# Optimization experiments

Measured on AMD Instinct MI355X. Metric: run time of the kernel, lower is better.

The kernel has to match this reference:

```python
import jax, jax.numpy as jnp
import numpy as np

# --- static config ---
B = 64        # graphs per batch
NPG = 512     # nodes per graph
N = B * NPG   # total nodes = 32768
EPG = 8192    # edges per graph (avg degree 16)
E = B * EPG   # total edges = 524288
L = 16        # tokens per node
V = 50000     # vocab
H = 256       # hidden_size == rnn hidden_size
P = 128       # projection_dim
K1 = 256      # ceil(0.5 * 512) nodes kept after pool 1
K2 = 128      # ceil(0.5 * 256) nodes kept after pool 2
PAD = 0


def setup_inputs() -> dict:
    key = jax.random.key(0)
    ks = jax.random.split(key, 16)
    tokens = jax.random.randint(ks[0], (N, L), 0, V, dtype=jnp.int32)
    eg = jnp.repeat(jnp.arange(B, dtype=jnp.int32), EPG)  # graph id per edge
    src = jax.random.randint(ks[1], (E,), 0, NPG, dtype=jnp.int32) + eg * NPG
    dst = jax.random.randint(ks[2], (E,), 0, NPG, dtype=jnp.int32) + eg * NPG
    edge_attr = jax.random.uniform(ks[3], (E, 2), dtype=jnp.float32)
    sH = 1.0 / np.sqrt(H).astype(np.float32)
    sP = 1.0 / np.sqrt(P).astype(np.float32)
    return {
        'tokens': tokens, 'src': src, 'dst': dst, 'edge_attr': edge_attr,
        'emb': jax.random.normal(ks[4], (V, H), jnp.float32) * 0.05,
        'W0': jax.random.normal(ks[5], (H, H), jnp.float32) * sH,
        'b0': jnp.zeros((H,), jnp.float32),
        'W1': jax.random.normal(ks[6], (H, H), jnp.float32) * sH,
        'b1': jnp.zeros((H,), jnp.float32),
        'p0': jax.random.normal(ks[7], (H,), jnp.float32),
        'p1': jax.random.normal(ks[8], (H,), jnp.float32),
        'wg': jax.random.normal(ks[9], (H, 1), jnp.float32) * sH,
        'bg': jnp.zeros((1,), jnp.float32),
        'Wp1': jax.random.normal(ks[10], (H, P), jnp.float32) * sH,
        'bp1': jnp.zeros((P,), jnp.float32),
        'Wp2': jax.random.normal(ks[11], (P, P), jnp.float32) * sP,
        'bp2': jnp.zeros((P,), jnp.float32),
    }


def _st_encode(tokens, emb):
    # STEncoder proxy: embed token ids, masked mean over non-pad tokens -> [N, H]
    mask = (tokens != PAD).astype(jnp.float32)  # [N, L]
    e = emb[tokens] * mask[..., None]           # [N, L, H]
    cnt = jnp.maximum(mask.sum(-1, keepdims=True), 1.0)
    return e.sum(1) / cnt


def _gcn(x, W, b, src, dst, w, n):
    # GCNConv with edge weights + self loops (fill 1), symmetric normalization
    h = x @ W                                        # [n, H]
    deg = jax.ops.segment_sum(w, dst, num_segments=n) + 1.0
    dinv = jax.lax.rsqrt(deg)
    norm = dinv[src] * w * dinv[dst]                 # [E]
    agg = jax.ops.segment_sum(h[src] * norm[:, None], dst, num_segments=n)
    return agg + h * (1.0 / deg)[:, None] + b


def _topk_pool(x, p, src, dst, w, n_per, k):
    # TopKPooling: score = x.p/||p||, keep top-k per graph, gate by tanh(score)
    G = x.shape[0] // n_per
    score = (x @ p) / jnp.linalg.norm(p)
    vals, idx = jax.lax.top_k(score.reshape(G, n_per), k)   # [G, k]
    perm = (idx + (jnp.arange(G, dtype=jnp.int32) * n_per)[:, None]).reshape(-1)
    x_new = x[perm] * jnp.tanh(vals.reshape(-1))[:, None]
    new_of_old = jnp.full((G * n_per,), -1, jnp.int32).at[perm].set(
        jnp.arange(G * k, dtype=jnp.int32))
    ns, nd = new_of_old[src], new_of_old[dst]
    keep = (ns >= 0) & (nd >= 0)
    # masked edges: weight 0 -> contribute nothing (== subgraph filtering)
    return (x_new, jnp.where(keep, ns, 0), jnp.where(keep, nd, 0),
            jnp.where(keep, w, 0.0))


def _attpool(x, wg, bg, k):
    # GlobalAttention: softmax(Linear(x,1)) over each graph's nodes
    G = x.shape[0] // k
    gate = (x @ wg + bg).reshape(G, k)        # [G, k]
    a = jax.nn.softmax(gate, axis=1)
    return jnp.einsum('gk,gkh->gh', a, x.reshape(G, k, x.shape[-1]))


def reference(tokens, src, dst, edge_attr, emb, W0, b0, W1, b1, p0, p1,
              wg, bg, Wp1, bp1, Wp2, bp2):
    w = edge_attr.mean(axis=1)                 # GCN path: scalar edge weights
    x = _st_encode(tokens, emb)                # [N, H]
    # layer 1
    x = jax.nn.relu(_gcn(x, W0, b0, src, dst, w, N))
    x, src1, dst1, w1 = _topk_pool(x, p0, src, dst, w, NPG, K1)
    out = _attpool(x, wg, bg, K1)              # [B, H]
    # hidden layer
    x = jax.nn.relu(_gcn(x, W1, b1, src1, dst1, w1, B * K1))
    x, _, _, _ = _topk_pool(x, p1, src1, dst1, w1, K1, K2)
    out = out + _attpool(x, wg, bg, K2)
    # projection head + L2 normalize
    h = jax.nn.relu(out @ Wp1 + bp1)
    logits = h @ Wp2 + bp2
    logits = logits / jnp.maximum(
        jnp.linalg.norm(logits, axis=-1, keepdims=True), 1e-12)
    return (logits, out)
```

## Files before the change

### kernel.cpp

```cpp
#include <hip/hip_runtime.h>
#include <hip/hip_bf16.h>

constexpr int C_B   = 64;
constexpr int C_NPG = 512;
constexpr int C_N   = 32768;
constexpr int C_E   = 524288;
constexpr int C_L   = 16;
constexpr int C_H   = 256;
constexpr int C_P   = 128;
constexpr int C_K1  = 256;
constexpr int C_K2  = 128;
constexpr int C_V   = 50000;

typedef __attribute__((ext_vector_type(8)))  short  short8;
typedef __attribute__((ext_vector_type(16))) float  float16;
typedef unsigned short ushort;
typedef unsigned int   uint;

__device__ inline void split_bf16(float x, ushort& h, ushort& l) {
    __hip_bfloat16 bh = __float2bfloat16(x);
    float fh = __bfloat162float(bh);
    __hip_bfloat16 bl = __float2bfloat16(x - fh);
    h = __builtin_bit_cast(ushort, bh);
    l = __builtin_bit_cast(ushort, bl);
}

__device__ inline ushort f2h(float x) {
    return __builtin_bit_cast(ushort, (_Float16)x);
}
__device__ inline float4 h4_to_f4(ushort4 v) {
    return make_float4((float)__builtin_bit_cast(_Float16, v.x),
                       (float)__builtin_bit_cast(_Float16, v.y),
                       (float)__builtin_bit_cast(_Float16, v.z),
                       (float)__builtin_bit_cast(_Float16, v.w));
}

template <int NPER>
__device__ inline void bitonic_desc(float& v, int& idx, float* svL, int* siL, int t) {
    #pragma unroll
    for (int k = 2; k <= NPER; k <<= 1) {
        bool desc = ((t & k) == 0);
        #pragma unroll
        for (int j = k >> 1; j > 0; j >>= 1) {
            bool amLo = ((t & j) == 0);
            bool keepMax = (desc == amLo);
            float pv; int pi;
            if (j >= 64) {
                __syncthreads();
                svL[t] = v; siL[t] = idx;
                __syncthreads();
                pv = svL[t ^ j]; pi = siL[t ^ j];
            } else {
                pv = __shfl_xor(v, j, 64);
                pi = __shfl_xor(idx, j, 64);
            }
            bool take = keepMax ? (pv > v) : (pv < v);
            if (take) { v = pv; idx = pi; }
        }
    }
}

__global__ void k_pre(const float* __restrict__ emb, ushort* __restrict__ emb16,
                      const float* __restrict__ ea, const int* __restrict__ dst,
                      float* __restrict__ w, float* __restrict__ degb, int* __restrict__ indegb,
                      const float* __restrict__ W0, const float* __restrict__ W1,
                      ushort* __restrict__ W0h, ushort* __restrict__ W0l,
                      ushort* __restrict__ W1h, ushort* __restrict__ W1l,
                      const float* __restrict__ p0, const float* __restrict__ p1,
                      float* __restrict__ invnp) {
    int b = blockIdx.x, t = threadIdx.x;
    __shared__ float r[256];
    if (b < 6250) {
        int i = (b * 256 + t) * 8;
        float4 a = *(const float4*)&emb[i];
        float4 c = *(const float4*)&emb[i + 4];
        short8 o;
        o[0] = (short)f2h(a.x); o[1] = (short)f2h(a.y);
        o[2] = (short)f2h(a.z); o[3] = (short)f2h(a.w);
        o[4] = (short)f2h(c.x); o[5] = (short)f2h(c.y);
        o[6] = (short)f2h(c.z); o[7] = (short)f2h(c.w);
        *(short8*)&emb16[i] = o;
    } else if (b < 8298) {
        int e = (b - 6250) * 256 + t;
        float ww = 0.5f * (ea[2 * e] + ea[2 * e + 1]);
        w[e] = ww;
        int d = dst[e];
        atomicAdd(&degb[d], ww);
        atomicAdd(&indegb[d], 1);
    } else if (b < 8810) {
        int g = (b - 8298) * 256 + t;
        int which = g >> 16;
        int idx = g & 65535;
        int k = idx >> 8, n = idx & 255;
        float x = (which ? W1 : W0)[idx];
        ushort h, l;
        split_bf16(x, h, l);
        size_t a = ((size_t)(n >> 5) * 16 + (k >> 4)) * 512 + ((k >> 3) & 1) * 256
                 + (n & 31) * 8 + (k & 7);
        if (which) { W1h[a] = h; W1l[a] = l; }
        else       { W0h[a] = h; W0l[a] = l; }
    } else {
        const float* p = (b == 8810) ? p0 : p1;
        float v = p[t];
        r[t] = v * v; __syncthreads();
        for (int s = 128; s; s >>= 1) { if (t < s) r[t] += r[t + s]; __syncthreads(); }
        if (t == 0) invnp[b - 8810] = rsqrtf(r[0]);
    }
}

template <int NPER>
__global__ void k_scan(const int* __restrict__ indeg, int* __restrict__ rowstart,
                       int* __restrict__ cursor, float* __restrict__ deg,
                       float* __restrict__ dinv) {
    int g = blockIdx.x, t = threadIdx.x;
    int node = g * NPER + t;
    float d = deg[node] + 1.f;
    dinv[node] = rsqrtf(d);
    deg[node]  = 1.f / d;
    __shared__ int s[NPER];
    int v = indeg[node];
    s[t] = v;
    __syncthreads();
    for (int off = 1; off < NPER; off <<= 1) {
        int add = (t >= off) ? s[t - off] : 0;
        __syncthreads();
        s[t] += add;
        __syncthreads();
    }
    int start = g * 8192 + s[t] - v;
    rowstart[node] = start;
    cursor[node]   = start;
}

__global__ void k_csr_scatter(const int* __restrict__ src, const int* __restrict__ dst,
                              const float* __restrict__ w, const float* __restrict__ dinv,
                              int* __restrict__ cursor, int* __restrict__ csr_src,
                              float* __restrict__ csr_nrm) {
    int e = blockIdx.x * blockDim.x + threadIdx.x;
    if (e >= C_E) return;
    int s = src[e], d = dst[e];
    int slot = atomicAdd(&cursor[d], 1);
    csr_src[slot] = s;
    csr_nrm[slot] = dinv[s] * w[e] * dinv[d];
}

__global__ __launch_bounds__(256)
void k_gcn_gather(const ushort* __restrict__ Hm, const int* __restrict__ rowstart,
                  const int* __restrict__ indeg, const int* __restrict__ csr_src,
                  const float* __restrict__ csr_nrm, const float* __restrict__ selfw,
                  const float* __restrict__ bias, const float* __restrict__ p,
                  const float* __restrict__ invnp, float* __restrict__ Xout,
                  float* __restrict__ score, int nnodes) {
    int n    = (blockIdx.x * blockDim.x + threadIdx.x) >> 6;
    int lane = threadIdx.x & 63;
    if (n >= nnodes) return;
    int h4 = lane * 4;
    float4 hv = h4_to_f4(*(const ushort4*)&Hm[(size_t)n * C_H + h4]);
    float  sw = selfw[n];
    float4 bv = *(const float4*)&bias[h4];
    float4 acc = make_float4(fmaf(hv.x, sw, bv.x), fmaf(hv.y, sw, bv.y),
                             fmaf(hv.z, sw, bv.z), fmaf(hv.w, sw, bv.w));
    int start = rowstart[n], cnt = indeg[n];
    const int*   sp = csr_src + start;
    const float* np = csr_nrm + start;
    #pragma unroll 4
    for (int j = 0; j < cnt; ++j) {
        int   s  = sp[j];
        float nm = np[j];
        float4 xv = h4_to_f4(*(const ushort4*)&Hm[(size_t)s * C_H + h4]);
        acc.x = fmaf(nm, xv.x, acc.x);
        acc.y = fmaf(nm, xv.y, acc.y);
        acc.z = fmaf(nm, xv.z, acc.z);
        acc.w = fmaf(nm, xv.w, acc.w);
    }
    acc.x = fmaxf(acc.x, 0.f); acc.y = fmaxf(acc.y, 0.f);
    acc.z = fmaxf(acc.z, 0.f); acc.w = fmaxf(acc.w, 0.f);
    *(float4*)&Xout[(size_t)n * C_H + h4] = acc;
    float4 pv = *(const float4*)&p[h4];
    float s = acc.x * pv.x + acc.y * pv.y + acc.z * pv.z + acc.w * pv.w;
    #pragma unroll
    for (int m = 32; m; m >>= 1) s += __shfl_xor(s, m, 64);
    if (lane == 0) score[n] = s * invnp[0];
}

__global__ __launch_bounds__(256)
void k_st_encode4(const int* __restrict__ tokens, const ushort* __restrict__ emb16,
                  ushort* __restrict__ Xh, ushort* __restrict__ Xl) {
    __shared__ float Xs[32 * 257];
    __shared__ int tokS[512];
    int tid = threadIdx.x;
    int blk = blockIdx.x;
    tokS[tid]       = tokens[(size_t)blk * 512 + tid];
    tokS[tid + 256] = tokens[(size_t)blk * 512 + tid + 256];
    __syncthreads();
    int w    = tid >> 6;
    int lane = tid & 63;
    for (int i = 0; i < 8; ++i) {
        int nl = w * 8 + i;
        float4 acc = make_float4(0.f, 0.f, 0.f, 0.f);
        int cnt = 0;
        #pragma unroll
        for (int t = 0; t < C_L; ++t) {
            int tk = tokS[nl * 16 + t];
            if (tk != 0) {
                float4 ev = h4_to_f4(*(const ushort4*)&emb16[(size_t)tk * C_H + lane * 4]);
                acc.x += ev.x; acc.y += ev.y; acc.z += ev.z; acc.w += ev.w;
                cnt++;
            }
        }
        float inv = 1.f / fmaxf((float)cnt, 1.f);
        float* xr = &Xs[nl * 257 + lane * 4];
        xr[0] = acc.x * inv; xr[1] = acc.y * inv;
        xr[2] = acc.z * inv; xr[3] = acc.w * inv;
    }
    __syncthreads();
    #pragma unroll
    for (int i = 0; i < 4; ++i) {
        int c    = tid + 256 * i;
        int kst  = c >> 6;
        int ln   = c & 63;
        int ml   = ln & 31;
        int kb   = kst * 16 + (ln >> 5) * 8;
        short8 hv, lv;
        #pragma unroll
        for (int j = 0; j < 8; ++j) {
            ushort h, l;
            split_bf16(Xs[ml * 257 + kb + j], h, l);
            hv[j] = (short)h; lv[j] = (short)l;
        }
        size_t base = (size_t)blk * 8192 + (size_t)c * 8;
        *(short8*)&Xh[base] = hv;
        *(short8*)&Xl[base] = lv;
    }
}

__global__ __launch_bounds__(256)
void k_gemm_mfma(const ushort* __restrict__ Ah, const ushort* __restrict__ Al,
                 const ushort* __restrict__ Bh, const ushort* __restrict__ Bl,
                 ushort* __restrict__ C) {
    __shared__ short lds[16384];
    int tid  = threadIdx.x;
    int lane = tid & 63;
    int wid  = tid >> 6;
    int wm   = wid & 1, wn = wid >> 1;
    int mb   = blockIdx.x;
    int nb   = blockIdx.y;

    float16 acc[2][2];
    #pragma unroll
    for (int mi = 0; mi < 2; ++mi)
        #pragma unroll
        for (int ni = 0; ni < 2; ++ni)
            #pragma unroll
            for (int r = 0; r < 16; ++r) acc[mi][ni][r] = 0.f;

    for (int kc = 0; kc < 8; ++kc) {
        __syncthreads();
        #pragma unroll
        for (int i = 0; i < 4; ++i) {
            int a  = tid + 256 * i;
            int s  = a >> 9;
            int mt = (a >> 7) & 3;
            int k2 = (a >> 6) & 1;
            int ln = a & 63;
            const ushort* ap = (s ? Al : Ah)
                + (((size_t)(mb * 4 + mt) * 16 + kc * 2 + k2) * 64 + ln) * 8;
            *(int4*)&lds[a * 8] = *(const int4*)ap;
            const ushort* bp = (s ? Bl : Bh)
                + (((size_t)(nb * 4 + mt) * 16 + kc * 2 + k2) * 64 + ln) * 8;
            *(int4*)&lds[8192 + a * 8] = *(const int4*)bp;
        }
        __syncthreads();
        #pragma unroll
        for (int k2 = 0; k2 < 2; ++k2) {
            short8 ah[2], al[2], bh[2], bl[2];
            #pragma unroll
            for (int mi = 0; mi < 2; ++mi) {
                int mt = wm * 2 + mi;
                ah[mi] = *(short8*)&lds[((mt * 2 + k2) * 64 + lane) * 8];
                al[mi] = *(short8*)&lds[(((4 + mt) * 2 + k2) * 64 + lane) * 8];
            }
            #pragma unroll
            for (int ni = 0; ni < 2; ++ni) {
                int nt = wn * 2 + ni;
                bh[ni] = *(short8*)&lds[8192 + ((nt * 2 + k2) * 64 + lane) * 8];
                bl[ni] = *(short8*)&lds[8192 + (((4 + nt) * 2 + k2) * 64 + lane) * 8];
            }
            #pragma unroll
            for (int mi = 0; mi < 2; ++mi)
                #pragma unroll
                for (int ni = 0; ni < 2; ++ni) {
                    acc[mi][ni] = __builtin_amdgcn_mfma_f32_32x32x16_bf16(
                        ah[mi], bh[ni], acc[mi][ni], 0, 0, 0);
                    acc[mi][ni] = __builtin_amdgcn_mfma_f32_32x32x16_bf16(
                        ah[mi], bl[ni], acc[mi][ni], 0, 0, 0);
                    acc[mi][ni] = __builtin_amdgcn_mfma_f32_32x32x16_bf16(
                        al[mi], bh[ni], acc[mi][ni], 0, 0, 0);
                }
        }
    }
    int col = lane & 31;
    int rquad = 4 * (lane >> 5);
    #pragma unroll
    for (int mi = 0; mi < 2; ++mi)
        #pragma unroll
        for (int ni = 0; ni < 2; ++ni) {
            int mbase = mb * 128 + wm * 64 + mi * 32;
            int nbase = nb * 128 + wn * 64 + ni * 32 + col;
            #pragma unroll
            for (int r = 0; r < 16; ++r) {
                int row = (r & 3) + 8 * (r >> 2) + rquad;
                C[(size_t)(mbase + row) * C_H + nbase] = f2h(acc[mi][ni][r]);
            }
        }
}

__global__ __launch_bounds__(512)
void k_pool1_fused(const float* __restrict__ score, const float* __restrict__ X,
                   const int* __restrict__ src, const int* __restrict__ dst,
                   const float* __restrict__ wbuf,
                   const float* __restrict__ wg, const float* __restrict__ bg,
                   ushort* __restrict__ XFh, ushort* __restrict__ XFl,
                   float* __restrict__ outb,
                   float* __restrict__ selfw1, int* __restrict__ rowst1,
                   int* __restrict__ indeg1, int* __restrict__ csrs,
                   float* __restrict__ csrn) {
    int g = blockIdx.x, t = threadIdx.x;
    int lane = t & 63, w = t >> 6;
    __shared__ float svL[C_NPG];
    __shared__ int   siL[C_NPG];
    __shared__ int   nooL[C_NPG];
    __shared__ int   olds[C_K1];
    __shared__ float gt[C_K1];
    __shared__ float sd[C_K1];
    __shared__ float red[C_K1];
    __shared__ float an[C_K1];
    __shared__ float wsum[8][C_H];
    __shared__ int   indegL[C_K1];
    __shared__ float degL[C_K1];
    __shared__ float dinvL[C_K1];
    __shared__ int   cursL[C_K1];

    float v = score[g * C_NPG + t];
    int   idx = t;
    bitonic_desc<C_NPG>(v, idx, svL, siL, t);
    __syncthreads();
    nooL[idx] = (t < C_K1) ? t : -1;
    if (t < C_K1) {
        olds[t]   = idx;
        gt[t]     = tanhf(v);
        indegL[t] = 0;
        degL[t]   = 0.f;
    }
    __syncthreads();

    float bgv = bg[0];
    {
        int r = t >> 1, half = t & 1;
        const float* xr = &X[(size_t)(g * C_NPG + olds[r]) * C_H + half * 128];
        const float* wr = &wg[half * 128];
        float s = 0.f;
        #pragma unroll
        for (int kk = 0; kk < 128; kk += 4) {
            float4 xv = *(const float4*)&xr[kk];
            float4 wv = *(const float4*)&wr[kk];
            s += xv.x * wv.x + xv.y * wv.y + xv.z * wv.z + xv.w * wv.w;
        }
        if (half) red[r] = s;
        __syncthreads();
        if (!half) sd[r] = gt[r] * (s + red[r]) + bgv;
        __syncthreads();
    }
    if (w == 0) {
        float m = fmaxf(fmaxf(sd[lane], sd[lane + 64]), fmaxf(sd[lane + 128], sd[lane + 192]));
        #pragma unroll
        for (int mm = 32; mm; mm >>= 1) m = fmaxf(m, __shfl_xor(m, mm, 64));
        if (lane == 0) red[0] = m;
    }
    __syncthreads();
    float mx = red[0];
    if (t < C_K1) an[t] = expf(sd[t] - mx);
    __syncthreads();
    if (w == 0) {
        float s4 = an[lane] + an[lane + 64] + an[lane + 128] + an[lane + 192];
        #pragma unroll
        for (int mm = 32; mm; mm >>= 1) s4 += __shfl_xor(s4, mm, 64);
        if (lane == 0) red[1] = s4;
    }
    __syncthreads();
    if (t < C_K1) an[t] = an[t] / red[1] * gt[t];
    __syncthreads();
    {
        float4 a4 = make_float4(0.f, 0.f, 0.f, 0.f);
        #pragma unroll 4
        for (int r = 0; r < 32; ++r) {
            int rr = w * 32 + r;
            float a = an[rr];
            float4 xv = *(const float4*)&X[(size_t)(g * C_NPG + olds[rr]) * C_H + lane * 4];
            a4.x = fmaf(a, xv.x, a4.x); a4.y = fmaf(a, xv.y, a4.y);
            a4.z = fmaf(a, xv.z, a4.z); a4.w = fmaf(a, xv.w, a4.w);
        }
        *(float4*)&wsum[w][lane * 4] = a4;
        __syncthreads();
        if (t < C_H) {
            float s = wsum[0][t] + wsum[1][t] + wsum[2][t] + wsum[3][t]
                    + wsum[4][t] + wsum[5][t] + wsum[6][t] + wsum[7][t];
            outb[g * C_H + t] = s;
        }
    }

    #pragma unroll
    for (int i = 0; i < 16; ++i) {
        int u   = t + 512 * i;
        int mt  = u >> 10;
        int c   = u & 1023;
        int kst = c >> 6, ln = c & 63, ml = ln & 31;
        int kb  = kst * 16 + (ln >> 5) * 8;
        int r   = mt * 32 + ml;
        const float* xp = &X[(size_t)(g * C_NPG + olds[r]) * C_H + kb];
        float gg = gt[r];
        float4 a = *(const float4*)&xp[0];
        float4 b = *(const float4*)&xp[4];
        float e8[8] = {a.x * gg, a.y * gg, a.z * gg, a.w * gg,
                       b.x * gg, b.y * gg, b.z * gg, b.w * gg};
        short8 hv, lv;
        #pragma unroll
        for (int j = 0; j < 8; ++j) {
            ushort h, l;
            split_bf16(e8[j], h, l);
            hv[j] = (short)h; lv[j] = (short)l;
        }
        size_t base = (size_t)(g * 8 + mt) * 8192 + (size_t)c * 8;
        *(short8*)&XFh[base] = hv;
        *(short8*)&XFl[base] = lv;
    }

    int   nsR[16], ndR[16];
    float wwR[16];
    #pragma unroll
    for (int i = 0; i < 16; ++i) {
        int e  = g * 8192 + t + 512 * i;
        int ns = nooL[src[e] - g * C_NPG];
        int nd = nooL[dst[e] - g * C_NPG];
        float ww = wbuf[e];
        nsR[i] = ns; ndR[i] = nd; wwR[i] = ww;
        if (ns >= 0 && nd >= 0) {
            atomicAdd(&indegL[nd], 1);
            unsafeAtomicAdd(&degL[nd], ww);
        }
    }
    __syncthreads();
    if (t < C_K1) {
        float d = degL[t] + 1.f;
        dinvL[t] = rsqrtf(d);
        selfw1[g * C_K1 + t] = 1.f / d;
        indeg1[g * C_K1 + t] = indegL[t];
    }
    if (w == 0) {
        int a0 = indegL[lane * 4], a1 = indegL[lane * 4 + 1];
        int a2 = indegL[lane * 4 + 2], a3 = indegL[lane * 4 + 3];
        int s4 = a0 + a1 + a2 + a3;
        int sc = s4;
        #pragma unroll
        for (int off = 1; off < 64; off <<= 1) {
            int pv = __shfl_up(sc, off, 64);
            if (lane >= off) sc += pv;
        }
        int base = g * 8192 + (sc - s4);
        cursL[lane * 4]     = base;
        cursL[lane * 4 + 1] = base + a0;
        cursL[lane * 4 + 2] = base + a0 + a1;
        cursL[lane * 4 + 3] = base + a0 + a1 + a2;
        rowst1[g * C_K1 + lane * 4]     = base;
        rowst1[g * C_K1 + lane * 4 + 1] = base + a0;
        rowst1[g * C_K1 + lane * 4 + 2] = base + a0 + a1;
        rowst1[g * C_K1 + lane * 4 + 3] = base + a0 + a1 + a2;
    }
    __syncthreads();
    #pragma unroll
    for (int i = 0; i < 16; ++i) {
        int ns = nsR[i], nd = ndR[i];
        if (ns >= 0 && nd >= 0) {
            int slot = atomicAdd(&cursL[nd], 1);
            csrs[slot] = g * C_K1 + ns;
            csrn[slot] = dinvL[ns] * wwR[i] * dinvL[nd];
        }
    }
}

__global__ __launch_bounds__(256)
void k_pool2_fused(const float* __restrict__ score, const float* __restrict__ X,
                   const float* __restrict__ wg, const float* __restrict__ bg,
                   float* __restrict__ outb) {
    int g = blockIdx.x, t = threadIdx.x;
    int lane = t & 63, w = t >> 6;
    __shared__ float svL[C_K1];
    __shared__ int   siL[C_K1];
    __shared__ int   olds[C_K2];
    __shared__ float gt[C_K2];
    __shared__ float sd[C_K2];
    __shared__ float red[C_K2];
    __shared__ float an[C_K2];
    __shared__ float wsum[4][C_H];

    float v = score[g * C_K1 + t];
    int   idx = t;
    bitonic_desc<C_K1>(v, idx, svL, siL, t);
    __syncthreads();
    if (t < C_K2) { olds[t] = idx; gt[t] = tanhf(v); }
    __syncthreads();

    float bgv = bg[0];
    {
        int r = t >> 1, half = t & 1;
        const float* xr = &X[(size_t)(g * C_K1 + olds[r]) * C_H + half * 128];
        const float* wr = &wg[half * 128];
        float s = 0.f;
        #pragma unroll
        for (int kk = 0; kk < 128; kk += 4) {
            float4 xv = *(const float4*)&xr[kk];
            float4 wv = *(const float4*)&wr[kk];
            s += xv.x * wv.x + xv.y * wv.y + xv.z * wv.z + xv.w * wv.w;
        }
        if (half) red[r] = s;
        __syncthreads();
        if (!half) sd[r] = gt[r] * (s + red[r]) + bgv;
        __syncthreads();
    }
    if (w == 0) {
        float m = fmaxf(sd[lane], sd[lane + 64]);
        #pragma unroll
        for (int mm = 32; mm; mm >>= 1) m = fmaxf(m, __shfl_xor(m, mm, 64));
        if (lane == 0) red[0] = m;
    }
    __syncthreads();
    float mx = red[0];
    if (t < C_K2) an[t] = expf(sd[t] - mx);
    __syncthreads();
    if (w == 0) {
        float s2 = an[lane] + an[lane + 64];
        #pragma unroll
        for (int mm = 32; mm; mm >>= 1) s2 += __shfl_xor(s2, mm, 64);
        if (lane == 0) red[1] = s2;
    }
    __syncthreads();
    if (t < C_K2) an[t] = an[t] / red[1] * gt[t];
    __syncthreads();
    {
        float4 a4 = make_float4(0.f, 0.f, 0.f, 0.f);
        #pragma unroll 4
        for (int r = 0; r < 32; ++r) {
            int rr = w * 32 + r;
            float a = an[rr];
            float4 xv = *(const float4*)&X[(size_t)(g * C_K1 + olds[rr]) * C_H + lane * 4];
            a4.x = fmaf(a, xv.x, a4.x); a4.y = fmaf(a, xv.y, a4.y);
            a4.z = fmaf(a, xv.z, a4.z); a4.w = fmaf(a, xv.w, a4.w);
        }
        *(float4*)&wsum[w][lane * 4] = a4;
        __syncthreads();
        float s = wsum[0][t] + wsum[1][t] + wsum[2][t] + wsum[3][t];
        outb[g * C_H + t] += s;
    }
}

__global__ void k_head(const float* __restrict__ outb, const float* __restrict__ Wp1,
                       const float* __restrict__ bp1, const float* __restrict__ Wp2,
                       const float* __restrict__ bp2, float* __restrict__ dout) {
    int g = blockIdx.x;
    int t = threadIdx.x;
    __shared__ float so[C_H];
    so[t] = outb[g * C_H + t];
    so[t + 128] = outb[g * C_H + t + 128];
    __syncthreads();
    float acc = bp1[t];
    for (int k = 0; k < C_H; ++k) acc += so[k] * Wp1[k * C_P + t];
    float hv = fmaxf(acc, 0.f);
    __shared__ float sh[C_P];
    sh[t] = hv; __syncthreads();
    float lg = bp2[t];
    for (int k = 0; k < C_P; ++k) lg += sh[k] * Wp2[k * C_P + t];
    __shared__ float red[C_P];
    red[t] = lg * lg; __syncthreads();
    for (int s = 64; s > 0; s >>= 1) { if (t < s) red[t] += red[t + s]; __syncthreads(); }
    float nrm = fmaxf(sqrtf(red[0]), 1e-12f);
    dout[g * C_P + t] = lg / nrm;
    dout[C_B * C_P + g * C_H + t]       = so[t];
    dout[C_B * C_P + g * C_H + t + 128] = so[t + 128];
}

extern "C" void kernel_launch(void* const* d_in, const int* in_sizes, int n_in,
                              void* d_out, int out_size, void* d_ws, size_t ws_size,
                              hipStream_t stream) {
    const int*   tokens = (const int*)d_in[0];
    const int*   src    = (const int*)d_in[1];
    const int*   dst    = (const int*)d_in[2];
    const float* eattr  = (const float*)d_in[3];
    const float* emb    = (const float*)d_in[4];
    const float* W0     = (const float*)d_in[5];
    const float* b0     = (const float*)d_in[6];
    const float* W1     = (const float*)d_in[7];
    const float* b1     = (const float*)d_in[8];
    const float* p0     = (const float*)d_in[9];
    const float* p1     = (const float*)d_in[10];
    const float* wg     = (const float*)d_in[11];
    const float* bg     = (const float*)d_in[12];
    const float* Wp1    = (const float*)d_in[13];
    const float* bp1    = (const float*)d_in[14];
    const float* Wp2    = (const float*)d_in[15];
    const float* bp2    = (const float*)d_in[16];
    float* out = (float*)d_out;

    float* f = (float*)d_ws;
    size_t o = 0;
    float*  XB    = f + o; o += (size_t)C_N * C_H;
    float*  HB    = f + o; o += (size_t)C_N * C_H;
    ushort* XFh   = (ushort*)(f + o); o += (size_t)C_N * C_H / 2;
    ushort* XFl   = (ushort*)(f + o); o += (size_t)C_N * C_H / 2;
    float*  wbuf  = f + o; o += C_E;
    float*  degb  = f + o; o += C_N;
    int*    indegb= (int*)(f + o); o += C_N;
    float*  dinv  = f + o; o += C_N;
    int*    rowst = (int*)(f + o); o += C_N;
    int*    curs  = (int*)(f + o); o += C_N;
    int*    csrs  = (int*)(f + o); o += C_E;
    float*  csrn  = f + o; o += C_E;
    float*  deg1  = f + o; o += C_B * C_K1;
    int*    indeg1= (int*)(f + o); o += C_B * C_K1;
    int*    rowst1= (int*)(f + o); o += C_B * C_K1;
    float*  outb  = f + o; o += C_B * C_H;
    float*  score = f + o; o += C_N;
    float*  invnp = f + o; o += 16;
    ushort* W0h   = (ushort*)(f + o); o += C_H * C_H / 2;
    ushort* W0l   = (ushort*)(f + o); o += C_H * C_H / 2;
    ushort* W1h   = (ushort*)(f + o); o += C_H * C_H / 2;
    ushort* W1l   = (ushort*)(f + o); o += C_H * C_H / 2;

    ushort* emb16 = (ushort*)XB;
    float*  AGG1  = XB;
    ushort* Hhf   = (ushort*)HB;

    hipMemsetAsync(degb, 0, 2 * C_N * sizeof(float), stream);

    k_pre<<<8812, 256, 0, stream>>>(emb, emb16, eattr, dst, wbuf, degb, indegb,
                                    W0, W1, W0h, W0l, W1h, W1l, p0, p1, invnp);
    k_st_encode4<<<C_N / 32, 256, 0, stream>>>(tokens, emb16, XFh, XFl);
    k_scan<C_NPG><<<C_B, C_NPG, 0, stream>>>(indegb, rowst, curs, degb, dinv);
    k_csr_scatter<<<C_E / 256, 256, 0, stream>>>(src, dst, wbuf, dinv, curs, csrs, csrn);

    k_gemm_mfma<<<dim3(C_N / 128, 2), 256, 0, stream>>>(XFh, XFl, W0h, W0l, Hhf);
    k_gcn_gather<<<(C_N * 64) / 256, 256, 0, stream>>>(
        Hhf, rowst, indegb, csrs, csrn, degb, b0, p0, invnp, XB, score, C_N);

    k_pool1_fused<<<C_B, 512, 0, stream>>>(
        score, XB, src, dst, wbuf, wg, bg, XFh, XFl, outb,
        deg1, rowst1, indeg1, csrs, csrn);

    k_gemm_mfma<<<dim3((C_B * C_K1) / 128, 2), 256, 0, stream>>>(XFh, XFl, W1h, W1l, Hhf);
    k_gcn_gather<<<(C_B * C_K1 * 64) / 256, 256, 0, stream>>>(
        Hhf, rowst1, indeg1, csrs, csrn, deg1, b1, p1, invnp + 1, AGG1, score, C_B * C_K1);

    k_pool2_fused<<<C_B, C_K1, 0, stream>>>(score, AGG1, wg, bg, outb);

    k_head<<<C_B, C_P, 0, stream>>>(outb, Wp1, bp1, Wp2, bp2, out);
}
```

Measured before the change: 375.3 us.

## Fuse launches and stage per-graph features in LDS for GCN aggregation

Merges the token encoder with the degree scan, and the first GEMM with the CSR scatter, into combined launches using block-index ranges. The GCN gather becomes a per-graph kernel that loads each graph's feature slice into LDS and aggregates neighbours from shared memory instead of global memory, writing partial scores per slice. The second-layer output is stored as fp16, and the pool2 and head kernels are fused. The aim is fewer launches and less scattered global traffic, at the cost of small grids (256 and 128 blocks) that may underuse the GPU, and extra rounding from fp16 storage.

```diff
diff --git a/kernel.cpp b/kernel.cpp
--- a/kernel.cpp
+++ b/kernel.cpp
@@ -28,11 +28,11 @@
 __device__ inline ushort f2h(float x) {
     return __builtin_bit_cast(ushort, (_Float16)x);
 }
+__device__ inline float h2f(ushort x) {
+    return (float)__builtin_bit_cast(_Float16, x);
+}
 __device__ inline float4 h4_to_f4(ushort4 v) {
-    return make_float4((float)__builtin_bit_cast(_Float16, v.x),
-                       (float)__builtin_bit_cast(_Float16, v.y),
-                       (float)__builtin_bit_cast(_Float16, v.z),
-                       (float)__builtin_bit_cast(_Float16, v.w));
+    return make_float4(h2f(v.x), h2f(v.y), h2f(v.z), h2f(v.w));
 }
 
 template <int NPER>
@@ -108,144 +108,93 @@
     }
 }
 
-template <int NPER>
-__global__ void k_scan(const int* __restrict__ indeg, int* __restrict__ rowstart,
-                       int* __restrict__ cursor, float* __restrict__ deg,
-                       float* __restrict__ dinv) {
-    int g = blockIdx.x, t = threadIdx.x;
-    int node = g * NPER + t;
-    float d = deg[node] + 1.f;
-    dinv[node] = rsqrtf(d);
-    deg[node]  = 1.f / d;
-    __shared__ int s[NPER];
-    int v = indeg[node];
-    s[t] = v;
-    __syncthreads();
-    for (int off = 1; off < NPER; off <<= 1) {
-        int add = (t >= off) ? s[t - off] : 0;
-        __syncthreads();
-        s[t] += add;
-        __syncthreads();
-    }
-    int start = g * 8192 + s[t] - v;
-    rowstart[node] = start;
-    cursor[node]   = start;
-}
-
-__global__ void k_csr_scatter(const int* __restrict__ src, const int* __restrict__ dst,
-                              const float* __restrict__ w, const float* __restrict__ dinv,
-                              int* __restrict__ cursor, int* __restrict__ csr_src,
-                              float* __restrict__ csr_nrm) {
-    int e = blockIdx.x * blockDim.x + threadIdx.x;
-    if (e >= C_E) return;
-    int s = src[e], d = dst[e];
-    int slot = atomicAdd(&cursor[d], 1);
-    csr_src[slot] = s;
-    csr_nrm[slot] = dinv[s] * w[e] * dinv[d];
-}
-
 __global__ __launch_bounds__(256)
-void k_gcn_gather(const ushort* __restrict__ Hm, const int* __restrict__ rowstart,
-                  const int* __restrict__ indeg, const int* __restrict__ csr_src,
-                  const float* __restrict__ csr_nrm, const float* __restrict__ selfw,
-                  const float* __restrict__ bias, const float* __restrict__ p,
-                  const float* __restrict__ invnp, float* __restrict__ Xout,
-                  float* __restrict__ score, int nnodes) {
-    int n    = (blockIdx.x * blockDim.x + threadIdx.x) >> 6;
-    int lane = threadIdx.x & 63;
-    if (n >= nnodes) return;
-    int h4 = lane * 4;
-    float4 hv = h4_to_f4(*(const ushort4*)&Hm[(size_t)n * C_H + h4]);
-    float  sw = selfw[n];
-    float4 bv = *(const float4*)&bias[h4];
-    float4 acc = make_float4(fmaf(hv.x, sw, bv.x), fmaf(hv.y, sw, bv.y),
-                             fmaf(hv.z, sw, bv.z), fmaf(hv.w, sw, bv.w));
-    int start = rowstart[n], cnt = indeg[n];
-    const int*   sp = csr_src + start;
-    const float* np = csr_nrm + start;
-    #pragma unroll 4
-    for (int j = 0; j < cnt; ++j) {
-        int   s  = sp[j];
-        float nm = np[j];
-        float4 xv = h4_to_f4(*(const ushort4*)&Hm[(size_t)s * C_H + h4]);
-        acc.x = fmaf(nm, xv.x, acc.x);
-        acc.y = fmaf(nm, xv.y, acc.y);
-        acc.z = fmaf(nm, xv.z, acc.z);
-        acc.w = fmaf(nm, xv.w, acc.w);
-    }
-    acc.x = fmaxf(acc.x, 0.f); acc.y = fmaxf(acc.y, 0.f);
-    acc.z = fmaxf(acc.z, 0.f); acc.w = fmaxf(acc.w, 0.f);
-    *(float4*)&Xout[(size_t)n * C_H + h4] = acc;
-    float4 pv = *(const float4*)&p[h4];
-    float s = acc.x * pv.x + acc.y * pv.y + acc.z * pv.z + acc.w * pv.w;
-    #pragma unroll
-    for (int m = 32; m; m >>= 1) s += __shfl_xor(s, m, 64);
-    if (lane == 0) score[n] = s * invnp[0];
-}
-
-__global__ __launch_bounds__(256)
-void k_st_encode4(const int* __restrict__ tokens, const ushort* __restrict__ emb16,
-                  ushort* __restrict__ Xh, ushort* __restrict__ Xl) {
-    __shared__ float Xs[32 * 257];
-    __shared__ int tokS[512];
-    int tid = threadIdx.x;
-    int blk = blockIdx.x;
-    tokS[tid]       = tokens[(size_t)blk * 512 + tid];
-    tokS[tid + 256] = tokens[(size_t)blk * 512 + tid + 256];
-    __syncthreads();
-    int w    = tid >> 6;
-    int lane = tid & 63;
-    for (int i = 0; i < 8; ++i) {
-        int nl = w * 8 + i;
-        float4 acc = make_float4(0.f, 0.f, 0.f, 0.f);
-        int cnt = 0;
-        #pragma unroll
-        for (int t = 0; t < C_L; ++t) {
-            int tk = tokS[nl * 16 + t];
-            if (tk != 0) {
-                float4 ev = h4_to_f4(*(const ushort4*)&emb16[(size_t)tk * C_H + lane * 4]);
-                acc.x += ev.x; acc.y += ev.y; acc.z += ev.z; acc.w += ev.w;
-                cnt++;
+void k_st_scan(const int* __restrict__ tokens, const ushort* __restrict__ emb16,
+               ushort* __restrict__ Xh, ushort* __restrict__ Xl,
+               const int* __restrict__ indeg, int* __restrict__ rowstart,
+               int* __restrict__ cursor, float* __restrict__ deg,
+               float* __restrict__ dinv) {
+    __shared__ float Xs[16 * 257];
+    __shared__ int tokS[256];
+    int blk = blockIdx.x, t = threadIdx.x;
+    if (blk < 2048) {
+        tokS[t] = tokens[(size_t)blk * 256 + t];
+        __syncthreads();
+        int w = t >> 6, lane = t & 63;
+        #pragma unroll
+        for (int i = 0; i < 4; ++i) {
+            int nl = w * 4 + i;
+            float4 acc = make_float4(0.f, 0.f, 0.f, 0.f);
+            int cnt = 0;
+            #pragma unroll
+            for (int tt = 0; tt < C_L; ++tt) {
+                int tk = tokS[nl * 16 + tt];
+                if (tk != 0) {
+                    float4 ev = h4_to_f4(*(const ushort4*)&emb16[(size_t)tk * C_H + lane * 4]);
+                    acc.x += ev.x; acc.y += ev.y; acc.z += ev.z; acc.w += ev.w;
+                    cnt++;
+                }
             }
-        }
-        float inv = 1.f / fmaxf((float)cnt, 1.f);
-        float* xr = &Xs[nl * 257 + lane * 4];
-        xr[0] = acc.x * inv; xr[1] = acc.y * inv;
-        xr[2] = acc.z * inv; xr[3] = acc.w * inv;
-    }
-    __syncthreads();
-    #pragma unroll
-    for (int i = 0; i < 4; ++i) {
-        int c    = tid + 256 * i;
-        int kst  = c >> 6;
-        int ln   = c & 63;
-        int ml   = ln & 31;
-        int kb   = kst * 16 + (ln >> 5) * 8;
-        short8 hv, lv;
-        #pragma unroll
-        for (int j = 0; j < 8; ++j) {
-            ushort h, l;
-            split_bf16(Xs[ml * 257 + kb + j], h, l);
-            hv[j] = (short)h; lv[j] = (short)l;
-        }
-        size_t base = (size_t)blk * 8192 + (size_t)c * 8;
-        *(short8*)&Xh[base] = hv;
-        *(short8*)&Xl[base] = lv;
-    }
-}
-
-__global__ __launch_bounds__(256)
-void k_gemm_mfma(const ushort* __restrict__ Ah, const ushort* __restrict__ Al,
-                 const ushort* __restrict__ Bh, const ushort* __restrict__ Bl,
-                 ushort* __restrict__ C) {
+            float inv = 1.f / fmaxf((float)cnt, 1.f);
+            float* xr = &Xs[nl * 257 + lane * 4];
+            xr[0] = acc.x * inv; xr[1] = acc.y * inv;
+            xr[2] = acc.z * inv; xr[3] = acc.w * inv;
+        }
+        __syncthreads();
+        int mtile = blk >> 1, rlo = (blk & 1) * 16;
+        #pragma unroll
+        for (int i = 0; i < 2; ++i) {
+            int u = t + 256 * i;
+            int kst = u >> 5, rr = u & 15, khalf = (u >> 4) & 1;
+            int kb = kst * 16 + khalf * 8;
+            int ln = khalf * 32 + rlo + rr;
+            short8 hv, lv;
+            #pragma unroll
+            for (int j = 0; j < 8; ++j) {
+                ushort h, l;
+                split_bf16(Xs[rr * 257 + kb + j], h, l);
+                hv[j] = (short)h; lv[j] = (short)l;
+            }
+            size_t base = (size_t)mtile * 8192 + ((size_t)kst * 64 + ln) * 8;
+            *(short8*)&Xh[base] = hv;
+            *(short8*)&Xl[base] = lv;
+        }
+    } else {
+        int g = blk - 2048;
+        if (t < 64) {
+            int lane = t;
+            int nodebase = g * C_NPG + lane * 8;
+            int a[8];
+            int tot = 0;
+            #pragma unroll
+            for (int i = 0; i < 8; ++i) { a[i] = indeg[nodebase + i]; tot += a[i]; }
+            int sc = tot;
+            #pragma unroll
+            for (int off = 1; off < 64; off <<= 1) {
+                int pv = __shfl_up(sc, off, 64);
+                if (lane >= off) sc += pv;
+            }
+            int run = g * 8192 + sc - tot;
+            #pragma unroll
+            for (int i = 0; i < 8; ++i) {
+                rowstart[nodebase + i] = run;
+                cursor[nodebase + i]   = run;
+                run += a[i];
+                float d = deg[nodebase + i] + 1.f;
+                dinv[nodebase + i] = rsqrtf(d);
+                deg[nodebase + i]  = 1.f / d;
+            }
+        }
+    }
+}
+
+__device__ inline void gemm_body(const ushort* __restrict__ Ah, const ushort* __restrict__ Al,
+                                 const ushort* __restrict__ Bh, const ushort* __restrict__ Bl,
+                                 ushort* __restrict__ C, int mb, int nb, int tid) {
     __shared__ short lds[16384];
-    int tid  = threadIdx.x;
     int lane = tid & 63;
     int wid  = tid >> 6;
     int wm   = wid & 1, wn = wid >> 1;
-    int mb   = blockIdx.x;
-    int nb   = blockIdx.y;
-
     float16 acc[2][2];
     #pragma unroll
     for (int mi = 0; mi < 2; ++mi)
@@ -253,7 +202,6 @@
         for (int ni = 0; ni < 2; ++ni)
             #pragma unroll
             for (int r = 0; r < 16; ++r) acc[mi][ni][r] = 0.f;
-
     for (int kc = 0; kc < 8; ++kc) {
         __syncthreads();
         #pragma unroll
@@ -315,8 +263,121 @@
         }
 }
 
+__global__ __launch_bounds__(256)
+void k_gemm1_csr(const ushort* __restrict__ Ah, const ushort* __restrict__ Al,
+                 const ushort* __restrict__ Bh, const ushort* __restrict__ Bl,
+                 ushort* __restrict__ C,
+                 const int* __restrict__ src, const int* __restrict__ dst,
+                 const float* __restrict__ wv, const float* __restrict__ dinv,
+                 int* __restrict__ cursor, int* __restrict__ csr_src,
+                 float* __restrict__ csr_nrm) {
+    int b = blockIdx.x, t = threadIdx.x;
+    if (b < 512) {
+        gemm_body(Ah, Al, Bh, Bl, C, b & 255, b >> 8, t);
+    } else {
+        int e = (b - 512) * 256 + t;
+        int s = src[e], d = dst[e];
+        int slot = atomicAdd(&cursor[d], 1);
+        csr_src[slot] = s;
+        csr_nrm[slot] = dinv[s] * wv[e] * dinv[d];
+    }
+}
+
+__global__ __launch_bounds__(256)
+void k_gemm_mfma(const ushort* __restrict__ Ah, const ushort* __restrict__ Al,
+                 const ushort* __restrict__ Bh, const ushort* __restrict__ Bl,
+                 ushort* __restrict__ C) {
+    gemm_body(Ah, Al, Bh, Bl, C, blockIdx.x, blockIdx.y, threadIdx.x);
+}
+
 __global__ __launch_bounds__(512)
-void k_pool1_fused(const float* __restrict__ score, const float* __restrict__ X,
+void k_gcn_lds1(const ushort* __restrict__ Hhf, const int* __restrict__ rowst,
+                const int* __restrict__ indeg, const int* __restrict__ csrs,
+                const float* __restrict__ csrn, const float* __restrict__ selfw,
+                const float* __restrict__ bias, const float* __restrict__ p,
+                float* __restrict__ Xout, float* __restrict__ scoreQ) {
+    __shared__ ushort Hs[C_NPG * 64];
+    int q = blockIdx.x, g = blockIdx.y, t = threadIdx.x;
+    int lane = t & 63, w = t >> 6;
+    #pragma unroll
+    for (int i = 0; i < 8; ++i) {
+        int u = t + 512 * i;
+        int r = u >> 3, uu = u & 7;
+        *(short8*)&Hs[r * 64 + uu * 8] =
+            *(const short8*)&Hhf[(size_t)(g * C_NPG + r) * C_H + q * 64 + uu * 8];
+    }
+    __syncthreads();
+    float bq = bias[q * 64 + lane];
+    float pq = p[q * 64 + lane];
+    for (int i = 0; i < 64; ++i) {
+        int nl = w * 64 + i;
+        int n  = g * C_NPG + nl;
+        float sw = selfw[n];
+        float acc = fmaf(h2f(Hs[nl * 64 + lane]), sw, bq);
+        int start = rowst[n], cnt = indeg[n];
+        #pragma unroll 4
+        for (int j = 0; j < cnt; ++j) {
+            int   s  = csrs[start + j] - g * C_NPG;
+            float nm = csrn[start + j];
+            acc = fmaf(nm, h2f(Hs[s * 64 + lane]), acc);
+        }
+        acc = fmaxf(acc, 0.f);
+        Xout[(size_t)n * C_H + q * 64 + lane] = acc;
+        float sc = acc * pq;
+        #pragma unroll
+        for (int m = 32; m; m >>= 1) sc += __shfl_xor(sc, m, 64);
+        if (lane == 0) scoreQ[q * C_N + n] = sc;
+    }
+}
+
+__global__ __launch_bounds__(512)
+void k_gcn_lds2(const ushort* __restrict__ Hhf, const int* __restrict__ rowst1,
+                const int* __restrict__ indeg1, const int* __restrict__ csrs,
+                const float* __restrict__ csrn, const float* __restrict__ selfw1,
+                const float* __restrict__ bias, const float* __restrict__ p,
+                ushort* __restrict__ Xtmp, float* __restrict__ scoreQ) {
+    __shared__ ushort Hs[C_K1 * 128];
+    int h = blockIdx.x, g = blockIdx.y, t = threadIdx.x;
+    int lane = t & 63, w = t >> 6;
+    #pragma unroll
+    for (int i = 0; i < 8; ++i) {
+        int u = t + 512 * i;
+        int r = u >> 4, uu = u & 15;
+        *(short8*)&Hs[r * 128 + uu * 8] =
+            *(const short8*)&Hhf[(size_t)(g * C_K1 + r) * C_H + h * 128 + uu * 8];
+    }
+    __syncthreads();
+    float2 bq = *(const float2*)&bias[h * 128 + lane * 2];
+    float2 pq = *(const float2*)&p[h * 128 + lane * 2];
+    for (int i = 0; i < 32; ++i) {
+        int nl = w * 32 + i;
+        int n  = g * C_K1 + nl;
+        float sw = selfw1[n];
+        ushort2 hv = *(const ushort2*)&Hs[nl * 128 + lane * 2];
+        float ax = fmaf(h2f(hv.x), sw, bq.x);
+        float ay = fmaf(h2f(hv.y), sw, bq.y);
+        int start = rowst1[n], cnt = indeg1[n];
+        #pragma unroll 4
+        for (int j = 0; j < cnt; ++j) {
+            int   s  = csrs[start + j] - g * C_K1;
+            float nm = csrn[start + j];
+            ushort2 xv = *(const ushort2*)&Hs[s * 128 + lane * 2];
+            ax = fmaf(nm, h2f(xv.x), ax);
+            ay = fmaf(nm, h2f(xv.y), ay);
+        }
+        ax = fmaxf(ax, 0.f); ay = fmaxf(ay, 0.f);
+        ushort2 o; o.x = f2h(ax); o.y = f2h(ay);
+        *(ushort2*)&Xtmp[(size_t)n * C_H + h * 128 + lane * 2] = o;
+        float sc = ax * pq.x + ay * pq.y;
+        #pragma unroll
+        for (int m = 32; m; m >>= 1) sc += __shfl_xor(sc, m, 64);
+        if (lane == 0) scoreQ[h * C_N + n] = sc;
+    }
+}
+
+__global__ __launch_bounds__(512)
+void k_pool1_fused(const float* __restrict__ scoreQ, const float* __restrict__ invnp,
+                   const float* __restrict__ X,
                    const int* __restrict__ src, const int* __restrict__ dst,
                    const float* __restrict__ wbuf,
                    const float* __restrict__ wg, const float* __restrict__ bg,
@@ -341,8 +402,10 @@
     __shared__ float dinvL[C_K1];
     __shared__ int   cursL[C_K1];
 
-    float v = score[g * C_NPG + t];
-    int   idx = t;
+    int t0 = g * C_NPG + t;
+    float v = (scoreQ[t0] + scoreQ[C_N + t0] + scoreQ[2 * C_N + t0] + scoreQ[3 * C_N + t0])
+              * invnp[0];
+    int idx = t;
     bitonic_desc<C_NPG>(v, idx, svL, siL, t);
     __syncthreads();
     nooL[idx] = (t < C_K1) ? t : -1;
@@ -489,9 +552,13 @@
 }
 
 __global__ __launch_bounds__(256)
-void k_pool2_fused(const float* __restrict__ score, const float* __restrict__ X,
-                   const float* __restrict__ wg, const float* __restrict__ bg,
-                   float* __restrict__ outb) {
+void k_pool2_head(const float* __restrict__ scoreQ, const float* __restrict__ invnp,
+                  const ushort* __restrict__ Xtmp,
+                  const float* __restrict__ wg, const float* __restrict__ bg,
+                  const float* __restrict__ outb,
+                  const float* __restrict__ Wp1, const float* __restrict__ bp1,
+                  const float* __restrict__ Wp2, const float* __restrict__ bp2,
+                  float* __restrict__ dout) {
     int g = blockIdx.x, t = threadIdx.x;
     int lane = t & 63, w = t >> 6;
     __shared__ float svL[C_K1];
@@ -499,12 +566,14 @@
     __shared__ int   olds[C_K2];
     __shared__ float gt[C_K2];
     __shared__ float sd[C_K2];
-    __shared__ float red[C_K2];
+    __shared__ float red2[C_K2];
     __shared__ float an[C_K2];
     __shared__ float wsum[4][C_H];
-
-    float v = score[g * C_K1 + t];
-    int   idx = t;
+    __shared__ float so[C_H];
+
+    int n0 = g * C_K1 + t;
+    float v = (scoreQ[n0] + scoreQ[C_N + n0]) * invnp[1];
+    int idx = t;
     bitonic_desc<C_K1>(v, idx, svL, siL, t);
     __syncthreads();
     if (t < C_K2) { olds[t] = idx; gt[t] = tanhf(v); }
@@ -513,38 +582,38 @@
     float bgv = bg[0];
     {
         int r = t >> 1, half = t & 1;
-        const float* xr = &X[(size_t)(g * C_K1 + olds[r]) * C_H + half * 128];
+        const ushort* xr = &Xtmp[(size_t)(g * C_K1 + olds[r]) * C_H + half * 128];
         const float* wr = &wg[half * 128];
         float s = 0.f;
         #pragma unroll
         for (int kk = 0; kk < 128; kk += 4) {
-            float4 xv = *(const float4*)&xr[kk];
+            float4 xv = h4_to_f4(*(const ushort4*)&xr[kk]);
             float4 wv = *(const float4*)&wr[kk];
             s += xv.x * wv.x + xv.y * wv.y + xv.z * wv.z + xv.w * wv.w;
         }
-        if (half) red[r] = s;
-        __syncthreads();
-        if (!half) sd[r] = gt[r] * (s + red[r]) + bgv;
+        if (half) red2[r] = s;
+        __syncthreads();
+        if (!half) sd[r] = gt[r] * (s + red2[r]) + bgv;
         __syncthreads();
     }
     if (w == 0) {
         float m = fmaxf(sd[lane], sd[lane + 64]);
         #pragma unroll
         for (int mm = 32; mm; mm >>= 1) m = fmaxf(m, __shfl_xor(m, mm, 64));
-        if (lane == 0) red[0] = m;
-    }
-    __syncthreads();
-    float mx = red[0];
+        if (lane == 0) red2[0] = m;
+    }
+    __syncthreads();
+    float mx = red2[0];
     if (t < C_K2) an[t] = expf(sd[t] - mx);
     __syncthreads();
     if (w == 0) {
         float s2 = an[lane] + an[lane + 64];
         #pragma unroll
         for (int mm = 32; mm; mm >>= 1) s2 += __shfl_xor(s2, mm, 64);
-        if (lane == 0) red[1] = s2;
-    }
-    __syncthreads();
-    if (t < C_K2) an[t] = an[t] / red[1] * gt[t];
+        if (lane == 0) red2[1] = s2;
+    }
+    __syncthreads();
+    if (t < C_K2) an[t] = an[t] / red2[1] * gt[t];
     __syncthreads();
     {
         float4 a4 = make_float4(0.f, 0.f, 0.f, 0.f);
@@ -552,40 +621,35 @@
         for (int r = 0; r < 32; ++r) {
             int rr = w * 32 + r;
             float a = an[rr];
-            float4 xv = *(const float4*)&X[(size_t)(g * C_K1 + olds[rr]) * C_H + lane * 4];
+            float4 xv = h4_to_f4(*(const ushort4*)&Xtmp[(size_t)(g * C_K1 + olds[rr]) * C_H + lane * 4]);
             a4.x = fmaf(a, xv.x, a4.x); a4.y = fmaf(a, xv.y, a4.y);
             a4.z = fmaf(a, xv.z, a4.z); a4.w = fmaf(a, xv.w, a4.w);
         }
         *(float4*)&wsum[w][lane * 4] = a4;
-        __syncthreads();
-        float s = wsum[0][t] + wsum[1][t] + wsum[2][t] + wsum[3][t];
-        outb[g * C_H + t] += s;
-    }
-}
-
-__global__ void k_head(const float* __restrict__ outb, const float* __restrict__ Wp1,
-                       const float* __restrict__ bp1, const float* __restrict__ Wp2,
-                       const float* __restrict__ bp2, float* __restrict__ dout) {
-    int g = blockIdx.x;
-    int t = threadIdx.x;
-    __shared__ float so[C_H];
-    so[t] = outb[g * C_H + t];
-    so[t + 128] = outb[g * C_H + t + 128];
-    __syncthreads();
-    float acc = bp1[t];
-    for (int k = 0; k < C_H; ++k) acc += so[k] * Wp1[k * C_P + t];
-    float hv = fmaxf(acc, 0.f);
-    __shared__ float sh[C_P];
-    sh[t] = hv; __syncthreads();
-    float lg = bp2[t];
-    for (int k = 0; k < C_P; ++k) lg += sh[k] * Wp2[k * C_P + t];
-    __shared__ float red[C_P];
-    red[t] = lg * lg; __syncthreads();
-    for (int s = 64; s > 0; s >>= 1) { if (t < s) red[t] += red[t + s]; __syncthreads(); }
-    float nrm = fmaxf(sqrtf(red[0]), 1e-12f);
-    dout[g * C_P + t] = lg / nrm;
-    dout[C_B * C_P + g * C_H + t]       = so[t];
-    dout[C_B * C_P + g * C_H + t + 128] = so[t + 128];
+    }
+    __syncthreads();
+    float o = outb[g * C_H + t] + wsum[0][t] + wsum[1][t] + wsum[2][t] + wsum[3][t];
+    so[t] = o;
+    dout[C_B * C_P + g * C_H + t] = o;
+    __syncthreads();
+
+    float lg = 0.f;
+    if (t < C_P) {
+        float acc = bp1[t];
+        for (int k = 0; k < C_H; ++k) acc += so[k] * Wp1[k * C_P + t];
+        float hv = fmaxf(acc, 0.f);
+        an[t] = hv;
+    }
+    __syncthreads();
+    if (t < C_P) {
+        lg = bp2[t];
+        for (int k = 0; k < C_P; ++k) lg += an[k] * Wp2[k * C_P + t];
+        red2[t] = lg * lg;
+    }
+    __syncthreads();
+    for (int s = 64; s; s >>= 1) { if (t < s) red2[t] += red2[t + s]; __syncthreads(); }
+    float nrm = fmaxf(sqrtf(red2[0]), 1e-12f);
+    if (t < C_P) dout[g * C_P + t] = lg / nrm;
 }
 
 extern "C" void kernel_launch(void* const* d_in, const int* in_sizes, int n_in,
@@ -628,7 +692,7 @@
     int*    indeg1= (int*)(f + o); o += C_B * C_K1;
     int*    rowst1= (int*)(f + o); o += C_B * C_K1;
     float*  outb  = f + o; o += C_B * C_H;
-    float*  score = f + o; o += C_N;
+    float*  scoreQ= f + o; o += 4 * (size_t)C_N;
     float*  invnp = f + o; o += 16;
     ushort* W0h   = (ushort*)(f + o); o += C_H * C_H / 2;
     ushort* W0l   = (ushort*)(f + o); o += C_H * C_H / 2;
@@ -636,30 +700,29 @@
     ushort* W1l   = (ushort*)(f + o); o += C_H * C_H / 2;
 
     ushort* emb16 = (ushort*)XB;
-    float*  AGG1  = XB;
     ushort* Hhf   = (ushort*)HB;
+    ushort* Xtmp  = (ushort*)XB;
 
     hipMemsetAsync(degb, 0, 2 * C_N * sizeof(float), stream);
 
     k_pre<<<8812, 256, 0, stream>>>(emb, emb16, eattr, dst, wbuf, degb, indegb,
                                     W0, W1, W0h, W0l, W1h, W1l, p0, p1, invnp);
-    k_st_encode4<<<C_N / 32, 256, 0, stream>>>(tokens, emb16, XFh, XFl);
-    k_scan<C_NPG><<<C_B, C_NPG, 0, stream>>>(indegb, rowst, curs, degb, dinv);
-    k_csr_scatter<<<C_E / 256, 256, 0, stream>>>(src, dst, wbuf, dinv, curs, csrs, csrn);
-
-    k_gemm_mfma<<<dim3(C_N / 128, 2), 256, 0, stream>>>(XFh, XFl, W0h, W0l, Hhf);
-    k_gcn_gather<<<(C_N * 64) / 256, 256, 0, stream>>>(
-        Hhf, rowst, indegb, csrs, csrn, degb, b0, p0, invnp, XB, score, C_N);
+    k_st_scan<<<2048 + C_B, 256, 0, stream>>>(tokens, emb16, XFh, XFl,
+                                              indegb, rowst, curs, degb, dinv);
+
+    k_gemm1_csr<<<512 + C_E / 256, 256, 0, stream>>>(
+        XFh, XFl, W0h, W0l, Hhf, src, dst, wbuf, dinv, curs, csrs, csrn);
+    k_gcn_lds1<<<dim3(4, C_B), 512, 0, stream>>>(
+        Hhf, rowst, indegb, csrs, csrn, degb, b0, p0, XB, scoreQ);
 
     k_pool1_fused<<<C_B, 512, 0, stream>>>(
-        score, XB, src, dst, wbuf, wg, bg, XFh, XFl, outb,
+        scoreQ, invnp, XB, src, dst, wbuf, wg, bg, XFh, XFl, outb,
         deg1, rowst1, indeg1, csrs, csrn);
 
     k_gemm_mfma<<<dim3((C_B * C_K1) / 128, 2), 256, 0, stream>>>(XFh, XFl, W1h, W1l, Hhf);
-    k_gcn_gather<<<(C_B * C_K1 * 64) / 256, 256, 0, stream>>>(
-        Hhf, rowst1, indeg1, csrs, csrn, deg1, b1, p1, invnp + 1, AGG1, score, C_B * C_K1);
-
-    k_pool2_fused<<<C_B, C_K1, 0, stream>>>(score, AGG1, wg, bg, outb);
-
-    k_head<<<C_B, C_P, 0, stream>>>(outb, Wp1, bp1, Wp2, bp2, out);
-}
+    k_gcn_lds2<<<dim3(2, C_B), 512, 0, stream>>>(
+        Hhf, rowst1, indeg1, csrs, csrn, deg1, b1, p1, Xtmp, scoreQ);
+
+    k_pool2_head<<<C_B, C_K1, 0, stream>>>(
+        scoreQ, invnp, Xtmp, wg, bg, outb, Wp1, bp1, Wp2, bp2, out);
+}
```

Result: slower. 459.1 us (+22.3%).
